# Optimization experiments

Hardware: AMD Instinct MI355X
Metric: run time of the kernel (lower is better)

## Reference

```python
import jax, jax.numpy as jnp
import numpy as np

EPS = 1e-8  # torch F.cosine_similarity eps


def setup_inputs() -> dict:
    key = jax.random.key(0)
    x = jax.random.normal(key, (16, 256, 2048), dtype=jnp.float32)
    return {"x": x}


def reference(x) -> jnp.ndarray:
    # x: [b, c, p]. Pairwise cosine similarity between point columns, diag = 1.
    # Equivalent to the original O(p) loop of F.cosine_similarity calls,
    # fused into one batched matmul.
    b, c, p = x.shape
    dots = jnp.einsum("bcp,bcq->bpq", x, x)            # [b, p, p]
    norms = jnp.sqrt(jnp.sum(x * x, axis=1))            # [b, p]
    denom = jnp.maximum(norms[:, :, None] * norms[:, None, :], EPS)
    sim = dots / denom
    eye = jnp.eye(p, dtype=x.dtype)
    res = jnp.where(eye[None, :, :] > 0, jnp.ones((), x.dtype), sim)
    return res
```

## Files before the change

kernel.cpp:

```cpp
#include <hip/hip_runtime.h>

#define B_ 16
#define C_ 256
#define P_ 2048
#define BK 32
#define NT_OFF 120

typedef __attribute__((ext_vector_type(8))) short short8;
typedef __attribute__((ext_vector_type(4))) float floatx4;

__device__ inline short f2bf(float v) {
  union { float f; unsigned u; } c; c.f = v;
  unsigned r = c.u + 0x7fffu + ((c.u >> 16) & 1u);
  return (short)(r >> 16);
}

#define GLOAD_LDS16(g, l)                                          \
  __builtin_amdgcn_global_load_lds(                                \
      (const __attribute__((address_space(1))) void*)(g),          \
      (__attribute__((address_space(3))) void*)(l), 16, 0, 0)

__global__ void k_transpose(const float* __restrict__ x, short* __restrict__ Xt,
                            float* __restrict__ nrm2) {
  __shared__ float t[32][33];
  __shared__ float red[8][32];
  const int p0 = blockIdx.x * 32, c0 = blockIdx.y * 32, b = blockIdx.z;
  const float* xb = x + (size_t)b * C_ * P_;
  short* xtb = Xt + (size_t)b * P_ * C_;
  const int tx = threadIdx.x, ty = threadIdx.y;
  float s = 0.f;
#pragma unroll
  for (int i = 0; i < 4; ++i) {
    float v = xb[(size_t)(c0 + ty + i * 8) * P_ + p0 + tx];
    t[ty + i * 8][tx] = v;
    s += v * v;
  }
  red[ty][tx] = s;
  __syncthreads();
  const int tid = ty * 32 + tx;
  const int r = tid >> 3;
  const int ch = tid & 7;
  short4 v;
  v.x = f2bf(t[ch * 4 + 0][r]);
  v.y = f2bf(t[ch * 4 + 1][r]);
  v.z = f2bf(t[ch * 4 + 2][r]);
  v.w = f2bf(t[ch * 4 + 3][r]);
  *reinterpret_cast<short4*>(&xtb[(size_t)(p0 + r) * C_ + c0 + ch * 4]) = v;
  if (tid < 32) {
    float ns = 0.f;
#pragma unroll
    for (int j = 0; j < 8; ++j) ns += red[j][tid];
    atomicAdd(&nrm2[b * P_ + p0 + tid], ns);
  }
}

__global__ __launch_bounds__(256, 3) void k_gemm(const short* __restrict__ Xt,
                                                 const float* __restrict__ nrm2,
                                                 float* __restrict__ out) {
  const int b = blockIdx.y;
  int t = blockIdx.x;
  int tm, tn;
  if (t < NT_OFF) {
    int rem = t, len = 15;
    tm = 0;
    while (rem >= len) { rem -= len; --len; ++tm; }
    tn = tm + 1 + rem;
  } else {
    tm = tn = t - NT_OFF;
  }
  const int p0 = tm * 128, q0 = tn * 128;
  const short* Xb = Xt + (size_t)b * P_ * C_;

  __shared__ __align__(16) short As[2][128 * BK];
  __shared__ __align__(16) short Bs[2][128 * BK];

  const int tid = threadIdx.x;
  const int lane = tid & 63;
  const int wid = tid >> 6;
  const int wrow = wid >> 1;
  const int wcol = wid & 1;

  floatx4 acc[4][4];
#pragma unroll
  for (int i = 0; i < 4; ++i)
#pragma unroll
    for (int j = 0; j < 4; ++j) acc[i][j] = (floatx4){0.f, 0.f, 0.f, 0.f};

  const int K2 = C_ * 2;

  auto STAGE = [&](int buf, int kt) {
    const int kb = kt * (BK * 2);
#pragma unroll
    for (int j = 0; j < 2; ++j) {
      const int chunk = j * 4 + wid;
      const int f = chunk * 1024 + lane * 16;
      const int row = f >> 6;
      const int inrow = f & 63;
      GLOAD_LDS16((const char*)Xb + (size_t)(p0 + row) * K2 + kb + inrow,
                  (char*)(&As[buf][0]) + chunk * 1024);
      GLOAD_LDS16((const char*)Xb + (size_t)(q0 + row) * K2 + kb + inrow,
                  (char*)(&Bs[buf][0]) + chunk * 1024);
    }
  };

  STAGE(0, 0);

  for (int kt = 0; kt < C_ / BK; ++kt) {
    const int cur = kt & 1;
    if (kt < C_ / BK - 1) {
      STAGE(cur ^ 1, kt + 1);
      asm volatile("s_waitcnt vmcnt(4)" ::: "memory");
    } else {
      asm volatile("s_waitcnt vmcnt(0)" ::: "memory");
    }
    __builtin_amdgcn_s_barrier();

    short8 af[4], bf[4];
#pragma unroll
    for (int mi = 0; mi < 4; ++mi) {
      const int r = wrow * 64 + mi * 16 + (lane & 15);
      af[mi] = *reinterpret_cast<const short8*>(&As[cur][r * BK + (lane >> 4) * 8]);
    }
#pragma unroll
    for (int ni = 0; ni < 4; ++ni) {
      const int r = wcol * 64 + ni * 16 + (lane & 15);
      bf[ni] = *reinterpret_cast<const short8*>(&Bs[cur][r * BK + (lane >> 4) * 8]);
    }
#pragma unroll
    for (int mi = 0; mi < 4; ++mi)
#pragma unroll
      for (int ni = 0; ni < 4; ++ni)
        acc[mi][ni] = __builtin_amdgcn_mfma_f32_16x16x32_bf16(bf[ni], af[mi], acc[mi][ni], 0, 0, 0);

    __builtin_amdgcn_s_barrier();
  }

  const float* n2 = nrm2 + (size_t)b * P_;
  float* ob = out + (size_t)b * P_ * P_;
  const int cl = lane & 15, ch4 = (lane >> 4) * 4;

  float rnp[4];
#pragma unroll
  for (int mi = 0; mi < 4; ++mi) {
    const int pr = p0 + wrow * 64 + mi * 16 + cl;
    rnp[mi] = __builtin_amdgcn_rcpf(fmaxf(sqrtf(n2[pr]), 1e-4f));
  }
  float rnq[4][4];
  int qb[4];
#pragma unroll
  for (int ni = 0; ni < 4; ++ni) {
    qb[ni] = q0 + wcol * 64 + ni * 16 + ch4;
    const float4 q2 = *reinterpret_cast<const float4*>(&n2[qb[ni]]);
    rnq[ni][0] = __builtin_amdgcn_rcpf(fmaxf(sqrtf(q2.x), 1e-4f));
    rnq[ni][1] = __builtin_amdgcn_rcpf(fmaxf(sqrtf(q2.y), 1e-4f));
    rnq[ni][2] = __builtin_amdgcn_rcpf(fmaxf(sqrtf(q2.z), 1e-4f));
    rnq[ni][3] = __builtin_amdgcn_rcpf(fmaxf(sqrtf(q2.w), 1e-4f));
  }

#pragma unroll
  for (int mi = 0; mi < 4; ++mi) {
    const int pr = p0 + wrow * 64 + mi * 16 + cl;
#pragma unroll
    for (int ni = 0; ni < 4; ++ni) {
      float4 v;
      v.x = acc[mi][ni][0] * rnp[mi] * rnq[ni][0];
      v.y = acc[mi][ni][1] * rnp[mi] * rnq[ni][1];
      v.z = acc[mi][ni][2] * rnp[mi] * rnq[ni][2];
      v.w = acc[mi][ni][3] * rnp[mi] * rnq[ni][3];
      if (tm == tn) {
        if (pr == qb[ni] + 0) v.x = 1.0f;
        if (pr == qb[ni] + 1) v.y = 1.0f;
        if (pr == qb[ni] + 2) v.z = 1.0f;
        if (pr == qb[ni] + 3) v.w = 1.0f;
      }
      *reinterpret_cast<float4*>(&ob[(size_t)pr * P_ + qb[ni]]) = v;
      if (tm != tn) {
        ob[(size_t)(qb[ni] + 0) * P_ + pr] = v.x;
        ob[(size_t)(qb[ni] + 1) * P_ + pr] = v.y;
        ob[(size_t)(qb[ni] + 2) * P_ + pr] = v.z;
        ob[(size_t)(qb[ni] + 3) * P_ + pr] = v.w;
      }
    }
  }
}

extern "C" void kernel_launch(void* const* d_in, const int* in_sizes, int n_in,
                              void* d_out, int out_size, void* d_ws, size_t ws_size,
                              hipStream_t stream) {
  const float* x = (const float*)d_in[0];
  float* out = (float*)d_out;

  short* Xt = (short*)d_ws;
  float* nrm2 = (float*)((char*)d_ws + (size_t)B_ * P_ * C_ * sizeof(short));

  hipMemsetAsync(nrm2, 0, (size_t)B_ * P_ * sizeof(float), stream);
  k_transpose<<<dim3(P_ / 32, C_ / 32, B_), dim3(32, 8), 0, stream>>>(x, Xt, nrm2);
  k_gemm<<<dim3(NT_OFF + P_ / 128, B_), 256, 0, stream>>>(Xt, nrm2, out);
}
```

Baseline: 99.53 us.

## Stage mirrored tile through LDS for coalesced transposed stores; remap blocks per XCD

Swaps the MFMA operand order so each lane holds a column of four rows, then writes the mirrored (transposed) tile through a per-wave LDS scratch buffer. This turns the previous scattered 4-byte transposed stores into float4 row stores. Block IDs are remapped so each XCD handles two whole batches, which is meant to improve L2 locality of the shared Xt rows. The direct-tile stores become four scalar row stores per fragment, and the kernel now uses 20KB more LDS, which may reduce occupancy.

```diff
diff --git a/kernel.cpp b/kernel.cpp
--- a/kernel.cpp
+++ b/kernel.cpp
@@ -4,6 +4,7 @@
 #define C_ 256
 #define P_ 2048
 #define BK 32
+#define NT 136
 #define NT_OFF 120
 
 typedef __attribute__((ext_vector_type(8))) short short8;
@@ -38,8 +39,7 @@
   red[ty][tx] = s;
   __syncthreads();
   const int tid = ty * 32 + tx;
-  const int r = tid >> 3;
-  const int ch = tid & 7;
+  const int r = tid >> 3, ch = tid & 7;
   short4 v;
   v.x = f2bf(t[ch * 4 + 0][r]);
   v.y = f2bf(t[ch * 4 + 1][r]);
@@ -57,8 +57,12 @@
 __global__ __launch_bounds__(256, 3) void k_gemm(const short* __restrict__ Xt,
                                                  const float* __restrict__ nrm2,
                                                  float* __restrict__ out) {
-  const int b = blockIdx.y;
-  int t = blockIdx.x;
+  const int bid = blockIdx.x;
+  const int xcd = bid & 7;
+  const int s = bid >> 3;
+  const int b = xcd * 2 + (s >= NT);
+  int t = s - (s >= NT ? NT : 0);
+
   int tm, tn;
   if (t < NT_OFF) {
     int rem = t, len = 15;
@@ -71,8 +75,8 @@
   const int p0 = tm * 128, q0 = tn * 128;
   const short* Xb = Xt + (size_t)b * P_ * C_;
 
-  __shared__ __align__(16) short As[2][128 * BK];
-  __shared__ __align__(16) short Bs[2][128 * BK];
+  __shared__ __align__(16) char smem[32768];
+  __shared__ __align__(16) float etile_s[4 * 1280];
 
   const int tid = threadIdx.x;
   const int lane = tid & 63;
@@ -97,9 +101,9 @@
       const int row = f >> 6;
       const int inrow = f & 63;
       GLOAD_LDS16((const char*)Xb + (size_t)(p0 + row) * K2 + kb + inrow,
-                  (char*)(&As[buf][0]) + chunk * 1024);
+                  smem + buf * 8192 + chunk * 1024);
       GLOAD_LDS16((const char*)Xb + (size_t)(q0 + row) * K2 + kb + inrow,
-                  (char*)(&Bs[buf][0]) + chunk * 1024);
+                  smem + 16384 + buf * 8192 + chunk * 1024);
     }
   };
 
@@ -109,76 +113,81 @@
     const int cur = kt & 1;
     if (kt < C_ / BK - 1) {
       STAGE(cur ^ 1, kt + 1);
-      asm volatile("s_waitcnt vmcnt(4)" ::: "memory");
+      asm volatile("s_waitcnt vmcnt(4)\n\ts_barrier" ::: "memory");
     } else {
-      asm volatile("s_waitcnt vmcnt(0)" ::: "memory");
-    }
-    __builtin_amdgcn_s_barrier();
-
+      asm volatile("s_waitcnt vmcnt(0)\n\ts_barrier" ::: "memory");
+    }
+
+    const short* As = (const short*)(smem + cur * 8192);
+    const short* Bs = (const short*)(smem + 16384 + cur * 8192);
     short8 af[4], bf[4];
 #pragma unroll
     for (int mi = 0; mi < 4; ++mi) {
       const int r = wrow * 64 + mi * 16 + (lane & 15);
-      af[mi] = *reinterpret_cast<const short8*>(&As[cur][r * BK + (lane >> 4) * 8]);
+      af[mi] = *reinterpret_cast<const short8*>(&As[r * BK + (lane >> 4) * 8]);
     }
 #pragma unroll
     for (int ni = 0; ni < 4; ++ni) {
       const int r = wcol * 64 + ni * 16 + (lane & 15);
-      bf[ni] = *reinterpret_cast<const short8*>(&Bs[cur][r * BK + (lane >> 4) * 8]);
+      bf[ni] = *reinterpret_cast<const short8*>(&Bs[r * BK + (lane >> 4) * 8]);
     }
 #pragma unroll
     for (int mi = 0; mi < 4; ++mi)
 #pragma unroll
       for (int ni = 0; ni < 4; ++ni)
-        acc[mi][ni] = __builtin_amdgcn_mfma_f32_16x16x32_bf16(bf[ni], af[mi], acc[mi][ni], 0, 0, 0);
-
-    __builtin_amdgcn_s_barrier();
+        acc[mi][ni] = __builtin_amdgcn_mfma_f32_16x16x32_bf16(af[mi], bf[ni], acc[mi][ni], 0, 0, 0);
+
+    asm volatile("s_waitcnt lgkmcnt(0)\n\ts_barrier" ::: "memory");
   }
 
   const float* n2 = nrm2 + (size_t)b * P_;
   float* ob = out + (size_t)b * P_ * P_;
-  const int cl = lane & 15, ch4 = (lane >> 4) * 4;
-
-  float rnp[4];
+  const int cl = lane & 15, rg4 = (lane >> 4) * 4;
+
+  float rnq[4];
+#pragma unroll
+  for (int ni = 0; ni < 4; ++ni) {
+    const int qc = q0 + wcol * 64 + ni * 16 + cl;
+    rnq[ni] = __builtin_amdgcn_rcpf(fmaxf(sqrtf(n2[qc]), 1e-4f));
+  }
+  floatx4 rnp[4];
 #pragma unroll
   for (int mi = 0; mi < 4; ++mi) {
-    const int pr = p0 + wrow * 64 + mi * 16 + cl;
-    rnp[mi] = __builtin_amdgcn_rcpf(fmaxf(sqrtf(n2[pr]), 1e-4f));
-  }
-  float rnq[4][4];
-  int qb[4];
-#pragma unroll
-  for (int ni = 0; ni < 4; ++ni) {
-    qb[ni] = q0 + wcol * 64 + ni * 16 + ch4;
-    const float4 q2 = *reinterpret_cast<const float4*>(&n2[qb[ni]]);
-    rnq[ni][0] = __builtin_amdgcn_rcpf(fmaxf(sqrtf(q2.x), 1e-4f));
-    rnq[ni][1] = __builtin_amdgcn_rcpf(fmaxf(sqrtf(q2.y), 1e-4f));
-    rnq[ni][2] = __builtin_amdgcn_rcpf(fmaxf(sqrtf(q2.z), 1e-4f));
-    rnq[ni][3] = __builtin_amdgcn_rcpf(fmaxf(sqrtf(q2.w), 1e-4f));
-  }
+    const float4 p2 = *reinterpret_cast<const float4*>(&n2[p0 + wrow * 64 + mi * 16 + rg4]);
+    rnp[mi][0] = __builtin_amdgcn_rcpf(fmaxf(sqrtf(p2.x), 1e-4f));
+    rnp[mi][1] = __builtin_amdgcn_rcpf(fmaxf(sqrtf(p2.y), 1e-4f));
+    rnp[mi][2] = __builtin_amdgcn_rcpf(fmaxf(sqrtf(p2.z), 1e-4f));
+    rnp[mi][3] = __builtin_amdgcn_rcpf(fmaxf(sqrtf(p2.w), 1e-4f));
+  }
+
+  float* etile = etile_s + wid * 1280;
 
 #pragma unroll
   for (int mi = 0; mi < 4; ++mi) {
-    const int pr = p0 + wrow * 64 + mi * 16 + cl;
+    const int prow = p0 + wrow * 64 + mi * 16 + rg4;
 #pragma unroll
     for (int ni = 0; ni < 4; ++ni) {
-      float4 v;
-      v.x = acc[mi][ni][0] * rnp[mi] * rnq[ni][0];
-      v.y = acc[mi][ni][1] * rnp[mi] * rnq[ni][1];
-      v.z = acc[mi][ni][2] * rnp[mi] * rnq[ni][2];
-      v.w = acc[mi][ni][3] * rnp[mi] * rnq[ni][3];
+      floatx4 vv = acc[mi][ni] * rnp[mi] * rnq[ni];
+      const int qc = q0 + wcol * 64 + ni * 16 + cl;
       if (tm == tn) {
-        if (pr == qb[ni] + 0) v.x = 1.0f;
-        if (pr == qb[ni] + 1) v.y = 1.0f;
-        if (pr == qb[ni] + 2) v.z = 1.0f;
-        if (pr == qb[ni] + 3) v.w = 1.0f;
+        const int d = qc - prow;
+        if (d >= 0 && d < 4) vv[d] = 1.0f;
       }
-      *reinterpret_cast<float4*>(&ob[(size_t)pr * P_ + qb[ni]]) = v;
-      if (tm != tn) {
-        ob[(size_t)(qb[ni] + 0) * P_ + pr] = v.x;
-        ob[(size_t)(qb[ni] + 1) * P_ + pr] = v.y;
-        ob[(size_t)(qb[ni] + 2) * P_ + pr] = v.z;
-        ob[(size_t)(qb[ni] + 3) * P_ + pr] = v.w;
+      ob[(size_t)(prow + 0) * P_ + qc] = vv[0];
+      ob[(size_t)(prow + 1) * P_ + qc] = vv[1];
+      ob[(size_t)(prow + 2) * P_ + qc] = vv[2];
+      ob[(size_t)(prow + 3) * P_ + qc] = vv[3];
+      if (tm != tn)
+        *reinterpret_cast<floatx4*>(&etile[(ni * 16 + cl) * 20 + rg4]) = vv;
+    }
+    if (tm != tn) {
+      const int pcb = p0 + wrow * 64 + mi * 16;
+#pragma unroll
+      for (int i = 0; i < 4; ++i) {
+        const int qq = i * 16 + (lane >> 2);
+        const floatx4 mv = *reinterpret_cast<const floatx4*>(&etile[qq * 20 + (lane & 3) * 4]);
+        *reinterpret_cast<floatx4*>(
+            &ob[(size_t)(q0 + wcol * 64 + qq) * P_ + pcb + (lane & 3) * 4]) = mv;
       }
     }
   }
@@ -195,5 +204,5 @@
 
   hipMemsetAsync(nrm2, 0, (size_t)B_ * P_ * sizeof(float), stream);
   k_transpose<<<dim3(P_ / 32, C_ / 32, B_), dim3(32, 8), 0, stream>>>(x, Xt, nrm2);
-  k_gemm<<<dim3(NT_OFF + P_ / 128, B_), 256, 0, stream>>>(Xt, nrm2, out);
-}
+  k_gemm<<<dim3(NT * B_), 256, 0, stream>>>(Xt, nrm2, out);
+}
```

Result: faster. 90.75 us (-8.8%).
